# Kernel tuning notes

Measured on AMD Instinct MI355X. Metric: run time of the kernel, lower is better.

Reference implementation:

```python
import jax, jax.numpy as jnp
import numpy as np

B, DIM, T, H = 8, 1024, 2048, 16
HD = DIM // H  # per-head channel dim = 64


def _toeplitz(v):
    # v: (H, T) -> (H, T, T) with M[h, i, j] = v[h, j - i] if j >= i else 0
    m = v.shape[-1]
    i = jnp.arange(m)[:, None]
    j = jnp.arange(m)[None, :]
    idx = jnp.where(j >= i, j - i, 0)
    return jnp.where(j >= i, v[..., idx], jnp.zeros((), v.dtype))


def setup_inputs() -> dict:
    key = jax.random.key(0)
    ks = jax.random.split(key, 5)
    s = 1.0 / np.sqrt(DIM)
    return {
        "x": jax.random.normal(ks[0], (B, DIM, T), jnp.float32),
        "w_in": jax.random.normal(ks[1], (DIM, DIM), jnp.float32) * s,
        "b_in": jnp.zeros((DIM,), jnp.float32),
        "w_out": jax.random.normal(ks[2], (DIM, DIM), jnp.float32) * s,
        "b_out": jnp.zeros((DIM,), jnp.float32),
        "toep_w": jax.random.normal(ks[3], (H, T), jnp.float32) * 0.02,
        "toep_b": jnp.zeros((H, T), jnp.float32),
    }


def reference(x, w_in, b_in, w_out, b_out, toep_w, toep_b):
    # x: (B, DIM, T) -> (B, T, DIM)
    xt = jnp.transpose(x, (0, 2, 1))
    h1 = xt @ w_in.T + b_in  # (B, T, DIM)
    # (B, T, H*HD) -> (B, H, HD, T)
    p = jnp.transpose(h1.reshape(B, T, H, HD), (0, 2, 3, 1))
    M = _toeplitz(toep_w)  # (H, T, T)
    # bmm with per-head causal Toeplitz matrix + per-head bias over time
    conv = jnp.einsum("bhdt,htu->bhdu", p, M) + toep_b[None, :, None, :]
    # (B, H, HD, T) -> (B, T, H*HD)
    merged = jnp.transpose(conv, (0, 3, 1, 2)).reshape(B, T, DIM)
    out = merged @ w_out.T + b_out  # (B, T, DIM)
    return jnp.transpose(out, (0, 2, 1))  # (B, DIM, T)
```

## Files before the change

kernel.cpp:

```cpp
#include <hip/hip_runtime.h>
#include <hip/hip_bf16.h>
#include <stdint.h>

#define B_   8
#define DIM  1024
#define T_   2048
#define H_   16
#define HD   64

typedef __attribute__((ext_vector_type(8))) short bf16x8;
typedef __attribute__((ext_vector_type(4))) float f32x4;
typedef __attribute__((ext_vector_type(4))) unsigned short u16x4;

__device__ __forceinline__ unsigned short f2bf(float f) {
    union { float f; unsigned u; } v{f};
    unsigned r = v.u + 0x7fffu + ((v.u >> 16) & 1u);
    return (unsigned short)(r >> 16);
}

__device__ __forceinline__ void gl_lds16(const unsigned short* g, unsigned short* l) {
    __builtin_amdgcn_global_load_lds(
        (const __attribute__((address_space(1))) void*)(const void*)g,
        (__attribute__((address_space(3))) void*)(void*)l,
        16, 0, 0);
}

__device__ __forceinline__ bf16x8 ld_frag(const unsigned short* smem, int row, int cg) {
    return *reinterpret_cast<const bf16x8*>(smem + row * 64 + (((cg) ^ (row & 7)) << 3));
}

__global__ void xpose_cast(const float* __restrict__ x, unsigned short* __restrict__ xt) {
    __shared__ float tile[64][65];
    const int b = blockIdx.z;
    const int d0 = blockIdx.y * 64, t0 = blockIdx.x * 64;
    const int tid = threadIdx.x;
    const int c = tid & 63;
    const int r0 = tid >> 6;

    const float* xp = x + ((size_t)b * DIM + d0) * T_ + t0;
#pragma unroll
    for (int i = 0; i < 16; ++i) {
        int r = r0 + i * 4;
        tile[r][c] = xp[(size_t)r * T_ + c];
    }
    __syncthreads();
    unsigned short* op = xt + ((size_t)b * T_ + t0) * DIM + d0;
    const int ci = (tid & 15) * 4;
    const int rr = tid >> 4;
#pragma unroll
    for (int i = 0; i < 4; ++i) {
        int r = rr + i * 16;
        u16x4 v;
#pragma unroll
        for (int j = 0; j < 4; ++j) v[j] = f2bf(tile[ci + j][r]);
        *reinterpret_cast<u16x4*>(op + (size_t)r * DIM + ci) = v;
    }
}

__global__ void cast_weights(const float* __restrict__ w_in, const float* __restrict__ w_out,
                             const float* __restrict__ tw,
                             unsigned short* __restrict__ w_in_b, unsigned short* __restrict__ w_out_b,
                             unsigned short* __restrict__ tw_b) {
    int i = blockIdx.x * 256 + threadIdx.x;
    if (i < DIM * DIM) {
        w_in_b[i]  = f2bf(w_in[i]);
        w_out_b[i] = f2bf(w_out[i]);
    }
    if (i < H_ * T_) tw_b[i] = f2bf(tw[i]);
}

__global__ void gen_mfrag(const unsigned short* __restrict__ twb, unsigned short* __restrict__ Mf) {
    const int h = blockIdx.y, dg = blockIdx.x;
    const int D = (dg - 1) * 64;
    unsigned short* out = Mf + (((size_t)h * 32 + dg) << 13);
    for (int v = threadIdx.x; v < 1024; v += 256) {
        int cg = v >> 7, row = v & 127;
        bf16x8 w;
#pragma unroll
        for (int j = 0; j < 8; ++j) {
            int lag = D + row - (cg * 8 + j);
            w[j] = (lag >= 0) ? (short)twb[h * T_ + lag] : (short)0;
        }
        *reinterpret_cast<bf16x8*>(out + (size_t)v * 8) = w;
    }
}

__global__ void gen_wfrag(const unsigned short* __restrict__ Wb, unsigned short* __restrict__ Wf) {
    const int kt = blockIdx.x, my = blockIdx.y;
    unsigned short* out = Wf + (((size_t)my * 16 + kt) << 13);
    for (int v = threadIdx.x; v < 1024; v += 256) {
        int cg = v >> 7, row = v & 127;
        bf16x8 w = *reinterpret_cast<const bf16x8*>(
            Wb + (size_t)(my * 128 + row) * DIM + kt * 64 + cg * 8);
        *reinterpret_cast<bf16x8*>(out + (size_t)v * 8) = w;
    }
}

template <bool OUT_BF16>
__global__ void gemm2_k(const unsigned short* __restrict__ Wf,
                        const unsigned short* __restrict__ Bm,
                        const float* __restrict__ bias,
                        void* __restrict__ Out) {
    __shared__ __align__(16) unsigned short Bs[2][128 * 64];

    const int flat = blockIdx.x;
    const int wid  = (flat & 7) * 128 + (flat >> 3);
    const int nx   = wid & 15;
    const int my   = (wid >> 4) & 7;
    const int b    = wid >> 7;

    const int tid = threadIdx.x, lane = tid & 63, wv = tid >> 6;
    const int m0 = my * 128;
    const int n0 = nx * 128;
    const unsigned short* Bb = Bm + (size_t)b * T_ * DIM + (size_t)n0 * DIM;
    const unsigned short* Aw = Wf + (((size_t)my * 16) << 13);

    const int wr = wv >> 1, wc = wv & 1;
    const int lrow = lane & 15, lg = lane >> 4;
    const int rsub = lane >> 3;
    const int g = (lane & 7) ^ rsub;

    const int aoff = (lg * 128 + wr * 64 + lrow) * 8;

    f32x4 acc[4][4] = {};

    auto BSTAGE = [&](int kt, int p) {
        const int k0 = kt * 64;
#pragma unroll
        for (int it = 0; it < 4; ++it) {
            int ch = wv * 4 + it;
            int r  = ch * 8 + rsub;
            gl_lds16(Bb + (size_t)r * DIM + k0 + g * 8, &Bs[p][0] + ch * 512);
        }
    };

    BSTAGE(0, 0);
    __syncthreads();

    const int NT = DIM / 64;
    for (int kt = 0; kt < NT; ++kt) {
        const int cur = kt & 1;
        if (kt + 1 < NT) BSTAGE(kt + 1, cur ^ 1);

        const unsigned short* At = Aw + ((size_t)kt << 13);
        bf16x8 af0[4], af1[4];
#pragma unroll
        for (int mt = 0; mt < 4; ++mt) {
            af0[mt] = *reinterpret_cast<const bf16x8*>(At + aoff + mt * 128);
            af1[mt] = *reinterpret_cast<const bf16x8*>(At + 4096 + aoff + mt * 128);
        }

        const unsigned short* Pb = &Bs[cur][0];
        bf16x8 bfr[4];
#pragma unroll
        for (int nt = 0; nt < 4; ++nt) bfr[nt] = ld_frag(Pb, wc * 64 + nt * 16 + lrow, lg);
#pragma unroll
        for (int mt = 0; mt < 4; ++mt)
#pragma unroll
            for (int nt = 0; nt < 4; ++nt)
                acc[mt][nt] = __builtin_amdgcn_mfma_f32_16x16x32_bf16(af0[mt], bfr[nt], acc[mt][nt], 0, 0, 0);
#pragma unroll
        for (int nt = 0; nt < 4; ++nt) bfr[nt] = ld_frag(Pb, wc * 64 + nt * 16 + lrow, 4 + lg);
#pragma unroll
        for (int mt = 0; mt < 4; ++mt)
#pragma unroll
            for (int nt = 0; nt < 4; ++nt)
                acc[mt][nt] = __builtin_amdgcn_mfma_f32_16x16x32_bf16(af1[mt], bfr[nt], acc[mt][nt], 0, 0, 0);

        __syncthreads();
    }

    const size_t ob = (size_t)b * DIM * T_;
#pragma unroll
    for (int mt = 0; mt < 4; ++mt) {
        int d = m0 + wr * 64 + mt * 16 + lg * 4;
#pragma unroll
        for (int nt = 0; nt < 4; ++nt) {
            int t = n0 + wc * 64 + nt * 16 + lrow;
#pragma unroll
            for (int r = 0; r < 4; ++r) {
                float v = acc[mt][nt][r] + bias[d + r];
                if constexpr (OUT_BF16)
                    ((unsigned short*)Out)[ob + (size_t)(d + r) * T_ + t] = f2bf(v);
                else
                    ((float*)Out)[ob + (size_t)(d + r) * T_ + t] = v;
            }
        }
    }
}

__global__ void conv4_k(const unsigned short* __restrict__ H1,
                        const unsigned short* __restrict__ Mf,
                        const float* __restrict__ tb,
                        unsigned short* __restrict__ Cb) {
    __shared__ __align__(16) unsigned short Ps[2][64 * 64];

    const int flat = blockIdx.x;
    const int wid  = (flat & 7) * 128 + (flat >> 3);
    const int bx   = wid & 7;
    const int b    = (wid >> 3) & 7;
    const int h    = wid >> 6;

    const int tid = threadIdx.x, lane = tid & 63, wv = tid >> 6;
    const unsigned short* Hb = H1 + ((size_t)b * DIM + h * HD) * T_;
    const unsigned short* Ah = Mf + ((size_t)h * 32) * 8192;

    const int lrow = lane & 15, lg = lane >> 4;
    const int rsub = lane >> 3;
    const int g = (lane & 7) ^ rsub;

    const int aoff = (lg * 128 + wv * 32 + lrow) * 8;

#pragma unroll
    for (int ph = 0; ph < 2; ++ph) {
        const int ut = ph ? bx : (T_ / 128 - 1 - bx);
        const int u0 = ut * 128;
        const int nk = 2 * ut + 2;
        f32x4 acc[2][4] = {};

#pragma unroll
        for (int it = 0; it < 2; ++it) {
            int ch = wv * 2 + it;
            int r  = ch * 8 + rsub;
            gl_lds16(Hb + (size_t)r * T_ + g * 8, &Ps[0][0] + ch * 512);
        }
        __syncthreads();

        for (int kt = 0; kt < nk; ++kt) {
            const int cur = kt & 1;
            if (kt + 1 < nk) {
                const int t0n = (kt + 1) * 64;
#pragma unroll
                for (int it = 0; it < 2; ++it) {
                    int ch = wv * 2 + it;
                    int r  = ch * 8 + rsub;
                    gl_lds16(Hb + (size_t)r * T_ + t0n + g * 8, &Ps[cur ^ 1][0] + ch * 512);
                }
            }
            const int dg = 2 * ut - kt + 1;
            const unsigned short* At = Ah + (size_t)dg * 8192;
            bf16x8 af0[2], af1[2];
#pragma unroll
            for (int mt = 0; mt < 2; ++mt) {
                af0[mt] = *reinterpret_cast<const bf16x8*>(At + aoff + mt * 128);
                af1[mt] = *reinterpret_cast<const bf16x8*>(At + 4096 + aoff + mt * 128);
            }
            const unsigned short* Pb = &Ps[cur][0];
            bf16x8 bfr[4];
#pragma unroll
            for (int nt = 0; nt < 4; ++nt) bfr[nt] = ld_frag(Pb, nt * 16 + lrow, lg);
#pragma unroll
            for (int mt = 0; mt < 2; ++mt)
#pragma unroll
                for (int nt = 0; nt < 4; ++nt)
                    acc[mt][nt] = __builtin_amdgcn_mfma_f32_16x16x32_bf16(af0[mt], bfr[nt], acc[mt][nt], 0, 0, 0);
#pragma unroll
            for (int nt = 0; nt < 4; ++nt) bfr[nt] = ld_frag(Pb, nt * 16 + lrow, 4 + lg);
#pragma unroll
            for (int mt = 0; mt < 2; ++mt)
#pragma unroll
                for (int nt = 0; nt < 4; ++nt)
                    acc[mt][nt] = __builtin_amdgcn_mfma_f32_16x16x32_bf16(af1[mt], bfr[nt], acc[mt][nt], 0, 0, 0);

            __syncthreads();
        }

        const size_t base = (size_t)b * T_ * DIM + (size_t)h * HD;
#pragma unroll
        for (int mt = 0; mt < 2; ++mt) {
            int u = u0 + wv * 32 + mt * 16 + lg * 4;
            const float* tbp = tb + h * T_ + u;
            float t0v = tbp[0], t1v = tbp[1], t2v = tbp[2], t3v = tbp[3];
#pragma unroll
            for (int nt = 0; nt < 4; ++nt) {
                int d = nt * 16 + lrow;
                size_t p = base + (size_t)u * DIM + d;
                Cb[p]           = f2bf(acc[mt][nt][0] + t0v);
                Cb[p + DIM]     = f2bf(acc[mt][nt][1] + t1v);
                Cb[p + 2 * DIM] = f2bf(acc[mt][nt][2] + t2v);
                Cb[p + 3 * DIM] = f2bf(acc[mt][nt][3] + t3v);
            }
        }
    }
}

extern "C" void kernel_launch(void* const* d_in, const int* in_sizes, int n_in,
                              void* d_out, int out_size, void* d_ws, size_t ws_size,
                              hipStream_t stream) {
    (void)in_sizes; (void)n_in; (void)out_size; (void)ws_size;
    const float* x      = (const float*)d_in[0];
    const float* w_in   = (const float*)d_in[1];
    const float* b_in   = (const float*)d_in[2];
    const float* w_out  = (const float*)d_in[3];
    const float* b_out  = (const float*)d_in[4];
    const float* toep_w = (const float*)d_in[5];
    const float* toep_b = (const float*)d_in[6];

    char* ws = (char*)d_ws;
    unsigned short* XT    = (unsigned short*)(ws);
    unsigned short* H1    = (unsigned short*)(ws + 33554432);
    unsigned short* Cbuf  = (unsigned short*)(ws + 67108864);
    unsigned short* winb  = (unsigned short*)(ws + 100663296);
    unsigned short* woutb = (unsigned short*)(ws + 102760448);
    unsigned short* twb   = (unsigned short*)(ws + 104857600);
    unsigned short* Mfrag = (unsigned short*)(ws + 104923136);
    unsigned short* WfI   = (unsigned short*)(ws + 113311744);
    unsigned short* WfO   = (unsigned short*)(ws + 115408896);

    xpose_cast<<<dim3(T_ / 64, DIM / 64, B_), dim3(256), 0, stream>>>(x, XT);
    cast_weights<<<dim3((DIM * DIM) / 256), dim3(256), 0, stream>>>(w_in, w_out, toep_w, winb, woutb, twb);
    gen_mfrag<<<dim3(32, H_), dim3(256), 0, stream>>>(twb, Mfrag);
    gen_wfrag<<<dim3(16, 8), dim3(256), 0, stream>>>(winb, WfI);
    gen_wfrag<<<dim3(16, 8), dim3(256), 0, stream>>>(woutb, WfO);
    gemm2_k<true><<<dim3(1024), dim3(256), 0, stream>>>(WfI, XT, b_in, (void*)H1);
    conv4_k<<<dim3(1024), dim3(256), 0, stream>>>(H1, Mfrag, toep_b, Cbuf);
    gemm2_k<false><<<dim3(1024), dim3(256), 0, stream>>>(WfO, Cbuf, b_out, d_out);
}
```

Baseline: 151.5 us.

## Fuse weight casts into fragment generators and single-buffer GEMM LDS tile

Removes the separate cast_weights kernel, so gen_mfrag and gen_wfrag read fp32 weights directly and convert them to bf16 inline. This drops one launch and an intermediate round trip through memory. The GEMM goes from double-buffered to single-buffered LDS: each K step issues its global-to-LDS load and then synchronizes before computing. That halves the LDS per block, which may allow more resident blocks, but it gives up overlap of loads with MFMA work within a block and adds a barrier per iteration.

```diff
diff --git a/kernel.cpp b/kernel.cpp
--- a/kernel.cpp
+++ b/kernel.cpp
@@ -57,21 +57,10 @@
     }
 }
 
-__global__ void cast_weights(const float* __restrict__ w_in, const float* __restrict__ w_out,
-                             const float* __restrict__ tw,
-                             unsigned short* __restrict__ w_in_b, unsigned short* __restrict__ w_out_b,
-                             unsigned short* __restrict__ tw_b) {
-    int i = blockIdx.x * 256 + threadIdx.x;
-    if (i < DIM * DIM) {
-        w_in_b[i]  = f2bf(w_in[i]);
-        w_out_b[i] = f2bf(w_out[i]);
-    }
-    if (i < H_ * T_) tw_b[i] = f2bf(tw[i]);
-}
-
-__global__ void gen_mfrag(const unsigned short* __restrict__ twb, unsigned short* __restrict__ Mf) {
+__global__ void gen_mfrag(const float* __restrict__ tw, unsigned short* __restrict__ Mf) {
     const int h = blockIdx.y, dg = blockIdx.x;
     const int D = (dg - 1) * 64;
+    const float* twh = tw + h * T_;
     unsigned short* out = Mf + (((size_t)h * 32 + dg) << 13);
     for (int v = threadIdx.x; v < 1024; v += 256) {
         int cg = v >> 7, row = v & 127;
@@ -79,29 +68,31 @@
 #pragma unroll
         for (int j = 0; j < 8; ++j) {
             int lag = D + row - (cg * 8 + j);
-            w[j] = (lag >= 0) ? (short)twb[h * T_ + lag] : (short)0;
+            w[j] = (lag >= 0) ? (short)f2bf(twh[lag]) : (short)0;
         }
         *reinterpret_cast<bf16x8*>(out + (size_t)v * 8) = w;
     }
 }
 
-__global__ void gen_wfrag(const unsigned short* __restrict__ Wb, unsigned short* __restrict__ Wf) {
+__global__ void gen_wfrag(const float* __restrict__ W, unsigned short* __restrict__ Wf) {
     const int kt = blockIdx.x, my = blockIdx.y;
     unsigned short* out = Wf + (((size_t)my * 16 + kt) << 13);
     for (int v = threadIdx.x; v < 1024; v += 256) {
         int cg = v >> 7, row = v & 127;
-        bf16x8 w = *reinterpret_cast<const bf16x8*>(
-            Wb + (size_t)(my * 128 + row) * DIM + kt * 64 + cg * 8);
+        const float* src = W + (size_t)(my * 128 + row) * DIM + kt * 64 + cg * 8;
+        bf16x8 w;
+#pragma unroll
+        for (int j = 0; j < 8; ++j) w[j] = (short)f2bf(src[j]);
         *reinterpret_cast<bf16x8*>(out + (size_t)v * 8) = w;
     }
 }
 
 template <bool OUT_BF16>
-__global__ void gemm2_k(const unsigned short* __restrict__ Wf,
+__global__ void gemm3_k(const unsigned short* __restrict__ Wf,
                         const unsigned short* __restrict__ Bm,
                         const float* __restrict__ bias,
                         void* __restrict__ Out) {
-    __shared__ __align__(16) unsigned short Bs[2][128 * 64];
+    __shared__ __align__(16) unsigned short Bs[128 * 64];
 
     const int flat = blockIdx.x;
     const int wid  = (flat & 7) * 128 + (flat >> 3);
@@ -124,24 +115,9 @@
 
     f32x4 acc[4][4] = {};
 
-    auto BSTAGE = [&](int kt, int p) {
-        const int k0 = kt * 64;
-#pragma unroll
-        for (int it = 0; it < 4; ++it) {
-            int ch = wv * 4 + it;
-            int r  = ch * 8 + rsub;
-            gl_lds16(Bb + (size_t)r * DIM + k0 + g * 8, &Bs[p][0] + ch * 512);
-        }
-    };
-
-    BSTAGE(0, 0);
-    __syncthreads();
-
     const int NT = DIM / 64;
     for (int kt = 0; kt < NT; ++kt) {
-        const int cur = kt & 1;
-        if (kt + 1 < NT) BSTAGE(kt + 1, cur ^ 1);
-
+        __syncthreads();
         const unsigned short* At = Aw + ((size_t)kt << 13);
         bf16x8 af0[4], af1[4];
 #pragma unroll
@@ -149,25 +125,32 @@
             af0[mt] = *reinterpret_cast<const bf16x8*>(At + aoff + mt * 128);
             af1[mt] = *reinterpret_cast<const bf16x8*>(At + 4096 + aoff + mt * 128);
         }
-
-        const unsigned short* Pb = &Bs[cur][0];
+        {
+            const int k0 = kt * 64;
+#pragma unroll
+            for (int it = 0; it < 4; ++it) {
+                int ch = wv * 4 + it;
+                int r  = ch * 8 + rsub;
+                gl_lds16(Bb + (size_t)r * DIM + k0 + g * 8, Bs + ch * 512);
+            }
+        }
+        __syncthreads();
+
         bf16x8 bfr[4];
 #pragma unroll
-        for (int nt = 0; nt < 4; ++nt) bfr[nt] = ld_frag(Pb, wc * 64 + nt * 16 + lrow, lg);
+        for (int nt = 0; nt < 4; ++nt) bfr[nt] = ld_frag(Bs, wc * 64 + nt * 16 + lrow, lg);
 #pragma unroll
         for (int mt = 0; mt < 4; ++mt)
 #pragma unroll
             for (int nt = 0; nt < 4; ++nt)
                 acc[mt][nt] = __builtin_amdgcn_mfma_f32_16x16x32_bf16(af0[mt], bfr[nt], acc[mt][nt], 0, 0, 0);
 #pragma unroll
-        for (int nt = 0; nt < 4; ++nt) bfr[nt] = ld_frag(Pb, wc * 64 + nt * 16 + lrow, 4 + lg);
+        for (int nt = 0; nt < 4; ++nt) bfr[nt] = ld_frag(Bs, wc * 64 + nt * 16 + lrow, 4 + lg);
 #pragma unroll
         for (int mt = 0; mt < 4; ++mt)
 #pragma unroll
             for (int nt = 0; nt < 4; ++nt)
                 acc[mt][nt] = __builtin_amdgcn_mfma_f32_16x16x32_bf16(af1[mt], bfr[nt], acc[mt][nt], 0, 0, 0);
-
-        __syncthreads();
     }
 
     const size_t ob = (size_t)b * DIM * T_;
@@ -300,19 +283,15 @@
     unsigned short* XT    = (unsigned short*)(ws);
     unsigned short* H1    = (unsigned short*)(ws + 33554432);
     unsigned short* Cbuf  = (unsigned short*)(ws + 67108864);
-    unsigned short* winb  = (unsigned short*)(ws + 100663296);
-    unsigned short* woutb = (unsigned short*)(ws + 102760448);
-    unsigned short* twb   = (unsigned short*)(ws + 104857600);
-    unsigned short* Mfrag = (unsigned short*)(ws + 104923136);
-    unsigned short* WfI   = (unsigned short*)(ws + 113311744);
-    unsigned short* WfO   = (unsigned short*)(ws + 115408896);
+    unsigned short* Mfrag = (unsigned short*)(ws + 100663296);
+    unsigned short* WfI   = (unsigned short*)(ws + 109051904);
+    unsigned short* WfO   = (unsigned short*)(ws + 111149056);
 
     xpose_cast<<<dim3(T_ / 64, DIM / 64, B_), dim3(256), 0, stream>>>(x, XT);
-    cast_weights<<<dim3((DIM * DIM) / 256), dim3(256), 0, stream>>>(w_in, w_out, toep_w, winb, woutb, twb);
-    gen_mfrag<<<dim3(32, H_), dim3(256), 0, stream>>>(twb, Mfrag);
-    gen_wfrag<<<dim3(16, 8), dim3(256), 0, stream>>>(winb, WfI);
-    gen_wfrag<<<dim3(16, 8), dim3(256), 0, stream>>>(woutb, WfO);
-    gemm2_k<true><<<dim3(1024), dim3(256), 0, stream>>>(WfI, XT, b_in, (void*)H1);
+    gen_mfrag<<<dim3(32, H_), dim3(256), 0, stream>>>(toep_w, Mfrag);
+    gen_wfrag<<<dim3(16, 8), dim3(256), 0, stream>>>(w_in, WfI);
+    gen_wfrag<<<dim3(16, 8), dim3(256), 0, stream>>>(w_out, WfO);
+    gemm3_k<true><<<dim3(1024), dim3(256), 0, stream>>>(WfI, XT, b_in, (void*)H1);
     conv4_k<<<dim3(1024), dim3(256), 0, stream>>>(H1, Mfrag, toep_b, Cbuf);
-    gemm2_k<false><<<dim3(1024), dim3(256), 0, stream>>>(WfO, Cbuf, b_out, d_out);
-}
+    gemm3_k<false><<<dim3(1024), dim3(256), 0, stream>>>(WfO, Cbuf, b_out, d_out);
+}
```

New measurement: 181.1 us. +19.6%, slower.
